# Performance work log

Hardware: AMD Instinct MI355X
Metric: run time of the kernel (lower is better)

Reference implementation:

```python
import jax, jax.numpy as jnp
import numpy as np

DIM = 512
HEADS = 8
HEAD_DIM = DIM // HEADS
MLP_HIDDEN = int(DIM * 4.0)
B, N = 4, 2048
LS_INIT = 1e-5
EPS = 1e-5


def _layernorm(x, w, b):
    mu = jnp.mean(x, axis=-1, keepdims=True)
    var = jnp.mean(jnp.square(x - mu), axis=-1, keepdims=True)
    return (x - mu) * jax.lax.rsqrt(var + EPS) * w + b


def setup_inputs() -> dict:
    key = jax.random.key(0)
    ks = jax.random.split(key, 12)
    s = 0.02
    return {
        "x": jax.random.normal(ks[0], (B, N, DIM), jnp.float32),
        "rel_pos_bias": jax.random.normal(ks[1], (HEADS, N, N), jnp.float32),
        "qkv_w": jax.random.normal(ks[2], (DIM, 3 * DIM), jnp.float32) * s,
        "qkv_b": jnp.zeros((3 * DIM,), jnp.float32),
        "out_w": jax.random.normal(ks[3], (DIM, DIM), jnp.float32) * s,
        "out_b": jnp.zeros((DIM,), jnp.float32),
        "ln1_w": jnp.ones((DIM,), jnp.float32),
        "ln1_b": jnp.zeros((DIM,), jnp.float32),
        "ln2_w": jnp.ones((DIM,), jnp.float32),
        "ln2_b": jnp.zeros((DIM,), jnp.float32),
        "ffn_w1": jax.random.normal(ks[4], (DIM, MLP_HIDDEN), jnp.float32) * s,
        "ffn_b1": jnp.zeros((MLP_HIDDEN,), jnp.float32),
        "ffn_w2": jax.random.normal(ks[5], (MLP_HIDDEN, DIM), jnp.float32) * s,
        "ffn_b2": jnp.zeros((DIM,), jnp.float32),
        "gamma1": jnp.full((DIM,), LS_INIT, jnp.float32),
        "gamma2": jnp.full((DIM,), LS_INIT, jnp.float32),
    }


def reference(x, rel_pos_bias, qkv_w, qkv_b, out_w, out_b, ln1_w, ln1_b,
              ln2_w, ln2_b, ffn_w1, ffn_b1, ffn_w2, ffn_b2, gamma1, gamma2):
    # Pre-norm MHA with relative-position bias
    y = _layernorm(x, ln1_w, ln1_b)                       # [B,N,C]
    qkv = y @ qkv_w + qkv_b                               # [B,N,3C]
    qkv = qkv.reshape(B, N, 3, HEADS, HEAD_DIM)
    q = jnp.transpose(qkv[:, :, 0], (0, 2, 1, 3))         # [B,H,N,D]
    k = jnp.transpose(qkv[:, :, 1], (0, 2, 1, 3))
    v = jnp.transpose(qkv[:, :, 2], (0, 2, 1, 3))
    scale = 1.0 / np.sqrt(HEAD_DIM).astype(np.float32)
    attn = jnp.einsum("bhid,bhjd->bhij", q, k) * scale    # [B,H,N,N]
    attn = attn + rel_pos_bias[None]
    attn = jax.nn.softmax(attn, axis=-1)
    out = jnp.einsum("bhij,bhjd->bhid", attn, v)          # [B,H,N,D]
    out = jnp.transpose(out, (0, 2, 1, 3)).reshape(B, N, DIM)
    out = out @ out_w + out_b
    x = x + out * gamma1                                  # layer scale, no drop-path (eval)
    # FFN with exact GELU
    y2 = _layernorm(x, ln2_w, ln2_b)
    h = jax.nn.gelu(y2 @ ffn_w1 + ffn_b1, approximate=False)
    ffn_out = h @ ffn_w2 + ffn_b2
    x = x + ffn_out * gamma2
    return x
```

## Files before the change

kernel.cpp:

```cpp
#include <hip/hip_runtime.h>
#include <hip/hip_bf16.h>
#include <math.h>

#define SEQ 2048
#define BATCH 4
#define DM 512
#define NH 8
#define HD 64
#define HID 2048
#define ROWS (BATCH * SEQ)

typedef __attribute__((ext_vector_type(8))) short short8;
typedef __attribute__((ext_vector_type(4))) float f32x4;

__device__ __forceinline__ short f2bf(float f) {
    unsigned u = __float_as_uint(f);
    u += 0x7fff + ((u >> 16) & 1);
    return (short)(u >> 16);
}

__device__ __forceinline__ void gl2lds16(const void* g, void* l) {
    __builtin_amdgcn_global_load_lds(
        (const __attribute__((address_space(1))) void*)g,
        (__attribute__((address_space(3))) void*)l, 16, 0, 0);
}

__global__ __launch_bounds__(256) void tcast_all(
    const float* __restrict__ qkv_w, const float* __restrict__ out_w,
    const float* __restrict__ w1, const float* __restrict__ w2,
    short* __restrict__ o_qkv, short* __restrict__ o_out,
    short* __restrict__ o_w1, short* __restrict__ o_w2) {
    __shared__ float tile[32][33];
    int id = blockIdx.x;
    const float* W; short* O; int K, N;
    if (id < 768)       { W = qkv_w; O = o_qkv; K = 512;  N = 1536; }
    else if (id < 1024) { W = out_w; O = o_out; K = 512;  N = 512;  id -= 768; }
    else if (id < 2048) { W = w1;    O = o_w1;  K = 512;  N = 2048; id -= 1024; }
    else                { W = w2;    O = o_w2;  K = 2048; N = 512;  id -= 2048; }
    int tn = N / 32;
    int n0 = (id % tn) * 32, k0 = (id / tn) * 32;
    int tx = threadIdx.x, ty = threadIdx.y;
#pragma unroll
    for (int i = 0; i < 4; ++i)
        tile[ty + i * 8][tx] = W[(size_t)(k0 + ty + i * 8) * N + n0 + tx];
    __syncthreads();
#pragma unroll
    for (int i = 0; i < 4; ++i)
        O[(size_t)(n0 + ty + i * 8) * K + k0 + tx] = f2bf(tile[tx][ty + i * 8]);
}

__global__ __launch_bounds__(256) void bias_prep(const float* __restrict__ bias,
                                                 short* __restrict__ biasP) {
    __shared__ short tl[16][1032];
    int t = threadIdx.x;
    int w = t >> 6, ln = t & 63, quad = ln >> 4, l15 = ln & 15;
    int id = blockIdx.x;
    int half = id & 1;
    int g = (id >> 1) & 127;
    int h = id >> 8;
    const float* src = bias + (size_t)h * SEQ * SEQ + (size_t)g * 16 * SEQ + half * 1024;
#pragma unroll
    for (int i = 0; i < 16; ++i) {
        float4 v = *(const float4*)(src + (size_t)i * SEQ + t * 4);
        float2 lo, hi;
        lo.x = v.x * 1.44269504f; lo.y = v.y * 1.44269504f;
        hi.x = v.z * 1.44269504f; hi.y = v.w * 1.44269504f;
        __hip_bfloat162 l2 = __float22bfloat162_rn(lo);
        __hip_bfloat162 h2 = __float22bfloat162_rn(hi);
        uint2 pp;
        pp.x = *(unsigned*)&l2;
        pp.y = *(unsigned*)&h2;
        *(uint2*)&tl[i][t * 4] = pp;
    }
    __syncthreads();
    int jtbase = half * 16;
#pragma unroll
    for (int u = 0; u < 4; ++u) {
        int jl = w * 4 + u;
        int tau = (h * 128 + g) * 32 + jtbase + jl;
#pragma unroll
        for (int n2 = 0; n2 < 2; ++n2) {
            uint2 a = *(const uint2*)&tl[l15][jl * 64 + n2 * 32 + quad * 4];
            uint2 b = *(const uint2*)&tl[l15][jl * 64 + n2 * 32 + 16 + quad * 4];
            uint4 pp;
            pp.x = a.x; pp.y = a.y; pp.z = b.x; pp.w = b.y;
            *(uint4*)(biasP + (size_t)tau * 1024 + n2 * 512 + ln * 8) = pp;
        }
    }
}

__global__ __launch_bounds__(256) void ln_k(const float* __restrict__ X,
                                            const float* __restrict__ g,
                                            const float* __restrict__ bta,
                                            short* __restrict__ Y) {
    int t = threadIdx.x;
    int wv = t >> 6, ln = t & 63;
    size_t row = (size_t)blockIdx.x * 4 + wv;
    const float* xr = X + row * DM;
    float4 v0 = *(const float4*)(xr + ln * 4);
    float4 v1 = *(const float4*)(xr + 256 + ln * 4);
    float s = v0.x + v0.y + v0.z + v0.w + v1.x + v1.y + v1.z + v1.w;
    float q = v0.x * v0.x + v0.y * v0.y + v0.z * v0.z + v0.w * v0.w +
              v1.x * v1.x + v1.y * v1.y + v1.z * v1.z + v1.w * v1.w;
#pragma unroll
    for (int off = 1; off < 64; off <<= 1) {
        s += __shfl_xor(s, off);
        q += __shfl_xor(q, off);
    }
    float mean = s * (1.0f / 512.0f);
    float var = q * (1.0f / 512.0f) - mean * mean;
    float rstd = rsqrtf(var + 1e-5f);
    int c0 = ln * 4, c1 = 256 + ln * 4;
    ushort4 o0, o1;
    o0.x = (unsigned short)f2bf((v0.x - mean) * rstd * g[c0 + 0] + bta[c0 + 0]);
    o0.y = (unsigned short)f2bf((v0.y - mean) * rstd * g[c0 + 1] + bta[c0 + 1]);
    o0.z = (unsigned short)f2bf((v0.z - mean) * rstd * g[c0 + 2] + bta[c0 + 2]);
    o0.w = (unsigned short)f2bf((v0.w - mean) * rstd * g[c0 + 3] + bta[c0 + 3]);
    o1.x = (unsigned short)f2bf((v1.x - mean) * rstd * g[c1 + 0] + bta[c1 + 0]);
    o1.y = (unsigned short)f2bf((v1.y - mean) * rstd * g[c1 + 1] + bta[c1 + 1]);
    o1.z = (unsigned short)f2bf((v1.z - mean) * rstd * g[c1 + 2] + bta[c1 + 2]);
    o1.w = (unsigned short)f2bf((v1.w - mean) * rstd * g[c1 + 3] + bta[c1 + 3]);
    *(ushort4*)((unsigned short*)Y + row * DM + c0) = o0;
    *(ushort4*)((unsigned short*)Y + row * DM + c1) = o1;
}

template <int EPI, int TN>
__global__ __launch_bounds__(256) void gemm_bt(const short* __restrict__ A,
                                               const short* __restrict__ Bt,
                                               const float* __restrict__ bias,
                                               const float* __restrict__ gamma,
                                               const float* __restrict__ res,
                                               void* __restrict__ Cout,
                                               short* __restrict__ Cout2,
                                               int M, int N, int K) {
    constexpr int NI = TN / 32;
    __shared__ __attribute__((aligned(16))) short As0[128][32];
    __shared__ __attribute__((aligned(16))) short As1[128][32];
    __shared__ __attribute__((aligned(16))) short Bs0[TN][32];
    __shared__ __attribute__((aligned(16))) short Bs1[TN][32];
    int t = threadIdx.x;
    int w = t >> 6, ln = t & 63;
    int quad = ln >> 4, l15 = ln & 15;
    int n0 = blockIdx.x * TN, m0 = blockIdx.y * 128;
    int wm = (w & 1) * 64, wn = (w >> 1) * (TN / 2);

    int srow0 = w * 32 + (ln >> 2);
    int srow1 = srow0 + 16;
    int srowB = w * 16 + (ln >> 2);
    int schunk = (ln & 3) * 8;
    const short* Ag0 = A + (size_t)(m0 + srow0) * K + schunk;
    const short* Ag1 = A + (size_t)(m0 + srow1) * K + schunk;
    const short* Bg0 = Bt + (size_t)(n0 + srow0) * K + schunk;
    const short* Bg1 = Bt + (size_t)(n0 + srow1) * K + schunk;
    const short* BgB = Bt + (size_t)(n0 + srowB) * K + schunk;

    f32x4 acc[4][NI];
#pragma unroll
    for (int i = 0; i < 4; ++i)
#pragma unroll
        for (int j = 0; j < NI; ++j) acc[i][j] = (f32x4){0.f, 0.f, 0.f, 0.f};

    for (int k0 = 0; k0 < K; k0 += 64) {
        __syncthreads();
        gl2lds16(Ag0 + k0, &As0[srow0][schunk]);
        gl2lds16(Ag1 + k0, &As0[srow1][schunk]);
        gl2lds16(Ag0 + k0 + 32, &As1[srow0][schunk]);
        gl2lds16(Ag1 + k0 + 32, &As1[srow1][schunk]);
        if (TN == 128) {
            gl2lds16(Bg0 + k0, &Bs0[srow0 & (TN - 1)][schunk]);
            gl2lds16(Bg1 + k0, &Bs0[srow1 & (TN - 1)][schunk]);
            gl2lds16(Bg0 + k0 + 32, &Bs1[srow0 & (TN - 1)][schunk]);
            gl2lds16(Bg1 + k0 + 32, &Bs1[srow1 & (TN - 1)][schunk]);
        } else {
            gl2lds16(BgB + k0, &Bs0[srowB & (TN - 1)][schunk]);
            gl2lds16(BgB + k0 + 32, &Bs1[srowB & (TN - 1)][schunk]);
        }
        __syncthreads();
        {
            short8 af[4], bf[NI];
#pragma unroll
            for (int mi = 0; mi < 4; ++mi)
                af[mi] = *(const short8*)&As0[wm + mi * 16 + l15][quad * 8];
#pragma unroll
            for (int ni = 0; ni < NI; ++ni)
                bf[ni] = *(const short8*)&Bs0[wn + ni * 16 + l15][quad * 8];
#pragma unroll
            for (int mi = 0; mi < 4; ++mi)
#pragma unroll
                for (int ni = 0; ni < NI; ++ni)
                    acc[mi][ni] = __builtin_amdgcn_mfma_f32_16x16x32_bf16(
                        af[mi], bf[ni], acc[mi][ni], 0, 0, 0);
        }
        {
            short8 af[4], bf[NI];
#pragma unroll
            for (int mi = 0; mi < 4; ++mi)
                af[mi] = *(const short8*)&As1[wm + mi * 16 + l15][quad * 8];
#pragma unroll
            for (int ni = 0; ni < NI; ++ni)
                bf[ni] = *(const short8*)&Bs1[wn + ni * 16 + l15][quad * 8];
#pragma unroll
            for (int mi = 0; mi < 4; ++mi)
#pragma unroll
                for (int ni = 0; ni < NI; ++ni)
                    acc[mi][ni] = __builtin_amdgcn_mfma_f32_16x16x32_bf16(
                        af[mi], bf[ni], acc[mi][ni], 0, 0, 0);
        }
    }

    if (EPI == 3 && n0 >= 1024) {
#pragma unroll
        for (int mi = 0; mi < 4; ++mi) {
#pragma unroll
            for (int ni = 0; ni < NI; ++ni) {
                int col = n0 + wn + ni * 16 + l15;
                int d = col - 1024, hh = d >> 6, dd = d & 63;
                int row0 = m0 + wm + mi * 16 + quad * 4;
                int bb = row0 >> 11, key = row0 & 2047;
                float bs = bias[col];
                ushort4 pk;
                pk.x = (unsigned short)f2bf(acc[mi][ni][0] + bs);
                pk.y = (unsigned short)f2bf(acc[mi][ni][1] + bs);
                pk.z = (unsigned short)f2bf(acc[mi][ni][2] + bs);
                pk.w = (unsigned short)f2bf(acc[mi][ni][3] + bs);
                *(ushort4*)&Cout2[((size_t)(bb * 8 + hh) * 64 + dd) * 2048 + key] = pk;
            }
        }
    } else {
#pragma unroll
        for (int mi = 0; mi < 4; ++mi) {
#pragma unroll
            for (int ni = 0; ni < NI; ++ni) {
#pragma unroll
                for (int r = 0; r < 4; ++r) {
                    int row = m0 + wm + mi * 16 + quad * 4 + r;
                    int col = n0 + wn + ni * 16 + l15;
                    float v = acc[mi][ni][r] + bias[col];
                    if (EPI == 0) {
                        ((short*)Cout)[(size_t)row * N + col] = f2bf(v);
                    } else if (EPI == 1) {
                        float u = v * fmaf(v * v, 0.0713548162f, 1.59576912f);
                        float gg = v / (1.0f + __expf(-u));
                        ((short*)Cout)[(size_t)row * N + col] = f2bf(gg);
                    } else if (EPI == 2) {
                        ((float*)Cout)[(size_t)row * N + col] =
                            fmaf(v, gamma[col], res[(size_t)row * N + col]);
                    } else {
                        float sc = (n0 < 512) ? 0.18033688f : 1.0f;
                        ((short*)Cout)[(size_t)row * 1024 + col] = f2bf(v * sc);
                    }
                }
            }
        }
    }
}

__global__ __launch_bounds__(256, 3) void attn_k(const short* __restrict__ qkv,
                                                 const short* __restrict__ vT,
                                                 const short* __restrict__ biasP,
                                                 short* __restrict__ Aout) {
    __shared__ __attribute__((aligned(16))) short Ks[2][64 * 64];
    __shared__ __attribute__((aligned(16))) short Vs[2][64 * 64];
    __shared__ __attribute__((aligned(16))) short Ps[4][2][16 * 64];
    int t = threadIdx.x;
    int w = t >> 6, ln = t & 63, quad = ln >> 4, l15 = ln & 15;
    int idx = blockIdx.x;
    int h = idx & 7, b = (idx >> 3) & 3, qt = idx >> 5;
    int qb = qt * 128 + w * 16;
    const size_t cbase = (size_t)b * SEQ * 1024;

    const short* qrow0 = qkv + cbase + (size_t)(qb + l15) * 1024 + h * 64;
    const short* qrow1 = qrow0 + (size_t)64 * 1024;
    short8 qf[2][2];
    qf[0][0] = *(const short8*)(qrow0 + quad * 8);
    qf[0][1] = *(const short8*)(qrow0 + 32 + quad * 8);
    qf[1][0] = *(const short8*)(qrow1 + quad * 8);
    qf[1][1] = *(const short8*)(qrow1 + 32 + quad * 8);

    int kr = t >> 3, kc = t & 7;
    int sc = (kc ^ (kr & 7)) * 8;
    const short* kgS = qkv + cbase + 512 + h * 64 + sc;
    const short* vgS = vT + (size_t)(b * 8 + h) * 64 * 2048 + sc;

    int g0 = qt * 8 + w;
    const short* bp0 = biasP + ((size_t)(h * 128 + g0) * 32) * 1024 + ln * 8;
    const short* bp1 = biasP + ((size_t)(h * 128 + g0 + 4) * 32) * 1024 + ln * 8;

    short8 ones;
#pragma unroll
    for (int i = 0; i < 8; ++i) ones[i] = (short)0x3F80;

    f32x4 o[2][4], ol[2];
#pragma unroll
    for (int qg = 0; qg < 2; ++qg) {
#pragma unroll
        for (int db = 0; db < 4; ++db) o[qg][db] = (f32x4){0.f, 0.f, 0.f, 0.f};
        ol[qg] = (f32x4){0.f, 0.f, 0.f, 0.f};
    }

    int sw7 = l15 & 7;

    gl2lds16(kgS,                              &Ks[0][t * 8]);
    gl2lds16(kgS + (size_t)32 * 1024,          &Ks[0][2048 + t * 8]);
    gl2lds16(vgS,                              &Vs[0][t * 8]);
    gl2lds16(vgS + (size_t)32 * 2048,          &Vs[0][2048 + t * 8]);
    uint4 bbc[2][2];
#pragma unroll
    for (int n2 = 0; n2 < 2; ++n2) {
        bbc[0][n2] = *(const uint4*)(bp0 + n2 * 512);
        bbc[1][n2] = *(const uint4*)(bp1 + n2 * 512);
    }

    int cur = 0;
    for (int jt = 0; jt < 32; ++jt) {
        __syncthreads();
        int jn = (jt < 31) ? (jt + 1) : jt;
        int j1 = jn * 64;
        int nxt = cur ^ 1;
        gl2lds16(kgS + (size_t)(j1 + kr) * 1024,      &Ks[nxt][t * 8]);
        gl2lds16(kgS + (size_t)(j1 + 32 + kr) * 1024, &Ks[nxt][2048 + t * 8]);
        gl2lds16(vgS + (size_t)kr * 2048 + j1,        &Vs[nxt][t * 8]);
        gl2lds16(vgS + (size_t)(32 + kr) * 2048 + j1, &Vs[nxt][2048 + t * 8]);

        f32x4 s4[2][4];
#pragma unroll
        for (int ni = 0; ni < 4; ++ni) {
            short8 k0 = *(const short8*)&Ks[cur][(ni * 16 + l15) * 64 + ((quad ^ sw7) * 8)];
            short8 k1 = *(const short8*)&Ks[cur][(ni * 16 + l15) * 64 + (((4 + quad) ^ sw7) * 8)];
#pragma unroll
            for (int qg = 0; qg < 2; ++qg) {
                uint4 bb = bbc[qg][ni >> 1];
                unsigned lo = (ni & 1) ? bb.z : bb.x;
                unsigned hi = (ni & 1) ? bb.w : bb.y;
                f32x4 z;
                z[0] = __uint_as_float(lo << 16);
                z[1] = __uint_as_float(lo & 0xffff0000u);
                z[2] = __uint_as_float(hi << 16);
                z[3] = __uint_as_float(hi & 0xffff0000u);
                z = __builtin_amdgcn_mfma_f32_16x16x32_bf16(k0, qf[qg][0], z, 0, 0, 0);
                s4[qg][ni] = __builtin_amdgcn_mfma_f32_16x16x32_bf16(k1, qf[qg][1], z, 0, 0, 0);
            }
        }
#pragma unroll
        for (int n2 = 0; n2 < 2; ++n2) {
            bbc[0][n2] = *(const uint4*)(bp0 + (size_t)jn * 1024 + n2 * 512);
            bbc[1][n2] = *(const uint4*)(bp1 + (size_t)jn * 1024 + n2 * 512);
        }
#pragma unroll
        for (int qg = 0; qg < 2; ++qg) {
#pragma unroll
            for (int ni = 0; ni < 4; ++ni) {
                float2 plo, phi;
                plo.x = exp2f(s4[qg][ni][0]);
                plo.y = exp2f(s4[qg][ni][1]);
                phi.x = exp2f(s4[qg][ni][2]);
                phi.y = exp2f(s4[qg][ni][3]);
                __hip_bfloat162 l2 = __float22bfloat162_rn(plo);
                __hip_bfloat162 h2 = __float22bfloat162_rn(phi);
                union { uint2 u; } pp;
                pp.u.x = *(unsigned*)&l2;
                pp.u.y = *(unsigned*)&h2;
                int c = ni * 2 + (quad >> 1);
                *(uint2*)&Ps[w][qg][l15 * 64 + ((c ^ sw7) * 8) + (quad & 1) * 4] = pp.u;
            }
        }
#pragma unroll
        for (int kk = 0; kk < 2; ++kk) {
            short8 ap0 = *(const short8*)&Ps[w][0][l15 * 64 + (((kk * 4 + quad) ^ sw7) * 8)];
            short8 ap1 = *(const short8*)&Ps[w][1][l15 * 64 + (((kk * 4 + quad) ^ sw7) * 8)];
#pragma unroll
            for (int db = 0; db < 4; ++db) {
                short8 vv = *(const short8*)&Vs[cur][(db * 16 + l15) * 64 + (((kk * 4 + quad) ^ sw7) * 8)];
                o[0][db] = __builtin_amdgcn_mfma_f32_16x16x32_bf16(ap0, vv, o[0][db], 0, 0, 0);
                o[1][db] = __builtin_amdgcn_mfma_f32_16x16x32_bf16(ap1, vv, o[1][db], 0, 0, 0);
            }
            ol[0] = __builtin_amdgcn_mfma_f32_16x16x32_bf16(ap0, ones, ol[0], 0, 0, 0);
            ol[1] = __builtin_amdgcn_mfma_f32_16x16x32_bf16(ap1, ones, ol[1], 0, 0, 0);
        }
        cur = nxt;
    }
#pragma unroll
    for (int qg = 0; qg < 2; ++qg) {
#pragma unroll
        for (int r = 0; r < 4; ++r) {
            float inv = 1.0f / ol[qg][r];
            int qrow_g = b * SEQ + qb + qg * 64 + quad * 4 + r;
#pragma unroll
            for (int db = 0; db < 4; ++db) {
                Aout[(size_t)qrow_g * DM + h * 64 + db * 16 + l15] =
                    f2bf(o[qg][db][r] * inv);
            }
        }
    }
}

extern "C" void kernel_launch(void* const* d_in, const int* in_sizes, int n_in,
                              void* d_out, int out_size, void* d_ws, size_t ws_size,
                              hipStream_t stream) {
    const float* x      = (const float*)d_in[0];
    const float* bias   = (const float*)d_in[1];
    const float* qkv_w  = (const float*)d_in[2];
    const float* qkv_b  = (const float*)d_in[3];
    const float* out_w  = (const float*)d_in[4];
    const float* out_b  = (const float*)d_in[5];
    const float* ln1_w  = (const float*)d_in[6];
    const float* ln1_b  = (const float*)d_in[7];
    const float* ln2_w  = (const float*)d_in[8];
    const float* ln2_b  = (const float*)d_in[9];
    const float* ffn_w1 = (const float*)d_in[10];
    const float* ffn_b1 = (const float*)d_in[11];
    const float* ffn_w2 = (const float*)d_in[12];
    const float* ffn_b2 = (const float*)d_in[13];
    const float* gamma1 = (const float*)d_in[14];
    const float* gamma2 = (const float*)d_in[15];
    float* out = (float*)d_out;

    short* wqkvT = (short*)d_ws;
    short* woutT = wqkvT + (size_t)1536 * 512;
    short* w1T   = woutT + (size_t)512 * 512;
    short* w2T   = w1T + (size_t)2048 * 512;
    short* y1    = w2T + (size_t)512 * 2048;
    short* qkvB  = y1 + (size_t)ROWS * DM;
    short* vTb   = qkvB + (size_t)ROWS * 1024;
    short* aoutB = vTb + (size_t)32 * 64 * 2048;
    float* x1    = (float*)(aoutB + (size_t)ROWS * DM);
    short* biasPw = (short*)(x1 + (size_t)ROWS * DM);
    short* hB    = qkvB;

    tcast_all<<<3072, dim3(32, 8), 0, stream>>>(qkv_w, out_w, ffn_w1, ffn_w2,
                                                wqkvT, woutT, w1T, w2T);
    bias_prep<<<2048, 256, 0, stream>>>(bias, biasPw);
    ln_k<<<ROWS / 4, 256, 0, stream>>>(x, ln1_w, ln1_b, y1);
    gemm_bt<3, 128><<<dim3(1536 / 128, ROWS / 128), 256, 0, stream>>>(
        y1, wqkvT, qkv_b, nullptr, nullptr, qkvB, vTb, ROWS, 1536, 512);
    attn_k<<<512, 256, 0, stream>>>(qkvB, vTb, biasPw, aoutB);
    gemm_bt<2, 64><<<dim3(512 / 64, ROWS / 128), 256, 0, stream>>>(
        aoutB, woutT, out_b, gamma1, x, x1, nullptr, ROWS, 512, 512);
    ln_k<<<ROWS / 4, 256, 0, stream>>>(x1, ln2_w, ln2_b, y1);
    gemm_bt<1, 128><<<dim3(2048 / 128, ROWS / 128), 256, 0, stream>>>(
        y1, w1T, ffn_b1, nullptr, nullptr, hB, nullptr, ROWS, 2048, 512);
    gemm_bt<2, 64><<<dim3(512 / 64, ROWS / 128), 256, 0, stream>>>(
        hB, w2T, ffn_b2, gamma2, x1, out, nullptr, ROWS, 512, 2048);
}
```

Baseline: 455.7 us.

## Merge bias preprocessing into QKV GEMM kernel via interleaved block roles

```diff
diff --git a/kernel.cpp b/kernel.cpp
--- a/kernel.cpp
+++ b/kernel.cpp
@@ -47,46 +47,6 @@
 #pragma unroll
     for (int i = 0; i < 4; ++i)
         O[(size_t)(n0 + ty + i * 8) * K + k0 + tx] = f2bf(tile[tx][ty + i * 8]);
-}
-
-__global__ __launch_bounds__(256) void bias_prep(const float* __restrict__ bias,
-                                                 short* __restrict__ biasP) {
-    __shared__ short tl[16][1032];
-    int t = threadIdx.x;
-    int w = t >> 6, ln = t & 63, quad = ln >> 4, l15 = ln & 15;
-    int id = blockIdx.x;
-    int half = id & 1;
-    int g = (id >> 1) & 127;
-    int h = id >> 8;
-    const float* src = bias + (size_t)h * SEQ * SEQ + (size_t)g * 16 * SEQ + half * 1024;
-#pragma unroll
-    for (int i = 0; i < 16; ++i) {
-        float4 v = *(const float4*)(src + (size_t)i * SEQ + t * 4);
-        float2 lo, hi;
-        lo.x = v.x * 1.44269504f; lo.y = v.y * 1.44269504f;
-        hi.x = v.z * 1.44269504f; hi.y = v.w * 1.44269504f;
-        __hip_bfloat162 l2 = __float22bfloat162_rn(lo);
-        __hip_bfloat162 h2 = __float22bfloat162_rn(hi);
-        uint2 pp;
-        pp.x = *(unsigned*)&l2;
-        pp.y = *(unsigned*)&h2;
-        *(uint2*)&tl[i][t * 4] = pp;
-    }
-    __syncthreads();
-    int jtbase = half * 16;
-#pragma unroll
-    for (int u = 0; u < 4; ++u) {
-        int jl = w * 4 + u;
-        int tau = (h * 128 + g) * 32 + jtbase + jl;
-#pragma unroll
-        for (int n2 = 0; n2 < 2; ++n2) {
-            uint2 a = *(const uint2*)&tl[l15][jl * 64 + n2 * 32 + quad * 4];
-            uint2 b = *(const uint2*)&tl[l15][jl * 64 + n2 * 32 + 16 + quad * 4];
-            uint4 pp;
-            pp.x = a.x; pp.y = a.y; pp.z = b.x; pp.w = b.y;
-            *(uint4*)(biasP + (size_t)tau * 1024 + n2 * 512 + ln * 8) = pp;
-        }
-    }
 }
 
 __global__ __launch_bounds__(256) void ln_k(const float* __restrict__ X,
@@ -208,48 +168,178 @@
         }
     }
 
-    if (EPI == 3 && n0 >= 1024) {
-#pragma unroll
-        for (int mi = 0; mi < 4; ++mi) {
-#pragma unroll
-            for (int ni = 0; ni < NI; ++ni) {
+#pragma unroll
+    for (int mi = 0; mi < 4; ++mi) {
+#pragma unroll
+        for (int ni = 0; ni < NI; ++ni) {
+#pragma unroll
+            for (int r = 0; r < 4; ++r) {
+                int row = m0 + wm + mi * 16 + quad * 4 + r;
                 int col = n0 + wn + ni * 16 + l15;
-                int d = col - 1024, hh = d >> 6, dd = d & 63;
-                int row0 = m0 + wm + mi * 16 + quad * 4;
-                int bb = row0 >> 11, key = row0 & 2047;
-                float bs = bias[col];
-                ushort4 pk;
-                pk.x = (unsigned short)f2bf(acc[mi][ni][0] + bs);
-                pk.y = (unsigned short)f2bf(acc[mi][ni][1] + bs);
-                pk.z = (unsigned short)f2bf(acc[mi][ni][2] + bs);
-                pk.w = (unsigned short)f2bf(acc[mi][ni][3] + bs);
-                *(ushort4*)&Cout2[((size_t)(bb * 8 + hh) * 64 + dd) * 2048 + key] = pk;
-            }
-        }
-    } else {
-#pragma unroll
-        for (int mi = 0; mi < 4; ++mi) {
-#pragma unroll
-            for (int ni = 0; ni < NI; ++ni) {
-#pragma unroll
-                for (int r = 0; r < 4; ++r) {
-                    int row = m0 + wm + mi * 16 + quad * 4 + r;
+                float v = acc[mi][ni][r] + bias[col];
+                if (EPI == 0) {
+                    ((short*)Cout)[(size_t)row * N + col] = f2bf(v);
+                } else if (EPI == 1) {
+                    float u = v * fmaf(v * v, 0.0713548162f, 1.59576912f);
+                    float gg = v / (1.0f + __expf(-u));
+                    ((short*)Cout)[(size_t)row * N + col] = f2bf(gg);
+                } else {
+                    ((float*)Cout)[(size_t)row * N + col] =
+                        fmaf(v, gamma[col], res[(size_t)row * N + col]);
+                }
+            }
+        }
+    }
+}
+
+__global__ __launch_bounds__(256) void qkvbias_k(
+    const short* __restrict__ A, const short* __restrict__ Bt,
+    const float* __restrict__ qkvb, short* __restrict__ Cout,
+    short* __restrict__ Cout2,
+    const float* __restrict__ bias, short* __restrict__ biasP) {
+    __shared__ __attribute__((aligned(16))) char smem[33024];
+    int bid = blockIdx.x;
+    int grp = bid / 11, sub = bid % 11;
+    int t = threadIdx.x;
+    int w = t >> 6, ln = t & 63;
+    int quad = ln >> 4, l15 = ln & 15;
+
+    if (sub < 3) {
+        typedef short (*tile32)[32];
+        tile32 As0 = (tile32)smem;
+        tile32 As1 = (tile32)(smem + 8192);
+        tile32 Bs0 = (tile32)(smem + 16384);
+        tile32 Bs1 = (tile32)(smem + 24576);
+        const int K = 512, N = 1536;
+        int g = grp * 3 + sub;
+        int n0 = (g % 12) * 128, m0 = (g / 12) * 128;
+        int wm = (w & 1) * 64, wn = (w >> 1) * 64;
+
+        int srow0 = w * 32 + (ln >> 2);
+        int srow1 = srow0 + 16;
+        int schunk = (ln & 3) * 8;
+        const short* Ag0 = A + (size_t)(m0 + srow0) * K + schunk;
+        const short* Ag1 = A + (size_t)(m0 + srow1) * K + schunk;
+        const short* Bg0 = Bt + (size_t)(n0 + srow0) * K + schunk;
+        const short* Bg1 = Bt + (size_t)(n0 + srow1) * K + schunk;
+
+        f32x4 acc[4][4];
+#pragma unroll
+        for (int i = 0; i < 4; ++i)
+#pragma unroll
+            for (int j = 0; j < 4; ++j) acc[i][j] = (f32x4){0.f, 0.f, 0.f, 0.f};
+
+        for (int k0 = 0; k0 < K; k0 += 64) {
+            __syncthreads();
+            gl2lds16(Ag0 + k0, &As0[srow0][schunk]);
+            gl2lds16(Ag1 + k0, &As0[srow1][schunk]);
+            gl2lds16(Ag0 + k0 + 32, &As1[srow0][schunk]);
+            gl2lds16(Ag1 + k0 + 32, &As1[srow1][schunk]);
+            gl2lds16(Bg0 + k0, &Bs0[srow0][schunk]);
+            gl2lds16(Bg1 + k0, &Bs0[srow1][schunk]);
+            gl2lds16(Bg0 + k0 + 32, &Bs1[srow0][schunk]);
+            gl2lds16(Bg1 + k0 + 32, &Bs1[srow1][schunk]);
+            __syncthreads();
+            {
+                short8 af[4], bf[4];
+#pragma unroll
+                for (int mi = 0; mi < 4; ++mi)
+                    af[mi] = *(const short8*)&As0[wm + mi * 16 + l15][quad * 8];
+#pragma unroll
+                for (int ni = 0; ni < 4; ++ni)
+                    bf[ni] = *(const short8*)&Bs0[wn + ni * 16 + l15][quad * 8];
+#pragma unroll
+                for (int mi = 0; mi < 4; ++mi)
+#pragma unroll
+                    for (int ni = 0; ni < 4; ++ni)
+                        acc[mi][ni] = __builtin_amdgcn_mfma_f32_16x16x32_bf16(
+                            af[mi], bf[ni], acc[mi][ni], 0, 0, 0);
+            }
+            {
+                short8 af[4], bf[4];
+#pragma unroll
+                for (int mi = 0; mi < 4; ++mi)
+                    af[mi] = *(const short8*)&As1[wm + mi * 16 + l15][quad * 8];
+#pragma unroll
+                for (int ni = 0; ni < 4; ++ni)
+                    bf[ni] = *(const short8*)&Bs1[wn + ni * 16 + l15][quad * 8];
+#pragma unroll
+                for (int mi = 0; mi < 4; ++mi)
+#pragma unroll
+                    for (int ni = 0; ni < 4; ++ni)
+                        acc[mi][ni] = __builtin_amdgcn_mfma_f32_16x16x32_bf16(
+                            af[mi], bf[ni], acc[mi][ni], 0, 0, 0);
+            }
+        }
+
+        if (n0 >= 1024) {
+#pragma unroll
+            for (int mi = 0; mi < 4; ++mi) {
+#pragma unroll
+                for (int ni = 0; ni < 4; ++ni) {
                     int col = n0 + wn + ni * 16 + l15;
-                    float v = acc[mi][ni][r] + bias[col];
-                    if (EPI == 0) {
-                        ((short*)Cout)[(size_t)row * N + col] = f2bf(v);
-                    } else if (EPI == 1) {
-                        float u = v * fmaf(v * v, 0.0713548162f, 1.59576912f);
-                        float gg = v / (1.0f + __expf(-u));
-                        ((short*)Cout)[(size_t)row * N + col] = f2bf(gg);
-                    } else if (EPI == 2) {
-                        ((float*)Cout)[(size_t)row * N + col] =
-                            fmaf(v, gamma[col], res[(size_t)row * N + col]);
-                    } else {
+                    int d = col - 1024, hh = d >> 6, dd = d & 63;
+                    int row0 = m0 + wm + mi * 16 + quad * 4;
+                    int bb = row0 >> 11, key = row0 & 2047;
+                    float bs = qkvb[col];
+                    ushort4 pk;
+                    pk.x = (unsigned short)f2bf(acc[mi][ni][0] + bs);
+                    pk.y = (unsigned short)f2bf(acc[mi][ni][1] + bs);
+                    pk.z = (unsigned short)f2bf(acc[mi][ni][2] + bs);
+                    pk.w = (unsigned short)f2bf(acc[mi][ni][3] + bs);
+                    *(ushort4*)&Cout2[((size_t)(bb * 8 + hh) * 64 + dd) * 2048 + key] = pk;
+                }
+            }
+        } else {
+#pragma unroll
+            for (int mi = 0; mi < 4; ++mi) {
+#pragma unroll
+                for (int ni = 0; ni < 4; ++ni) {
+#pragma unroll
+                    for (int r = 0; r < 4; ++r) {
+                        int row = m0 + wm + mi * 16 + quad * 4 + r;
+                        int col = n0 + wn + ni * 16 + l15;
+                        float v = acc[mi][ni][r] + qkvb[col];
                         float sc = (n0 < 512) ? 0.18033688f : 1.0f;
-                        ((short*)Cout)[(size_t)row * 1024 + col] = f2bf(v * sc);
+                        Cout[(size_t)row * 1024 + col] = f2bf(v * sc);
                     }
                 }
+            }
+        }
+    } else {
+        typedef short (*tile1032)[1032];
+        tile1032 tl = (tile1032)smem;
+        int id = grp * 8 + (sub - 3);
+        int half = id & 1;
+        int g = (id >> 1) & 127;
+        int h = id >> 8;
+        const float* src = bias + (size_t)h * SEQ * SEQ + (size_t)g * 16 * SEQ + half * 1024;
+#pragma unroll
+        for (int i = 0; i < 16; ++i) {
+            float4 v = *(const float4*)(src + (size_t)i * SEQ + t * 4);
+            float2 lo, hi;
+            lo.x = v.x * 1.44269504f; lo.y = v.y * 1.44269504f;
+            hi.x = v.z * 1.44269504f; hi.y = v.w * 1.44269504f;
+            __hip_bfloat162 l2 = __float22bfloat162_rn(lo);
+            __hip_bfloat162 h2 = __float22bfloat162_rn(hi);
+            uint2 pp;
+            pp.x = *(unsigned*)&l2;
+            pp.y = *(unsigned*)&h2;
+            *(uint2*)&tl[i][t * 4] = pp;
+        }
+        __syncthreads();
+        int jtbase = half * 16;
+#pragma unroll
+        for (int u = 0; u < 4; ++u) {
+            int jl = w * 4 + u;
+            int tau = (h * 128 + g) * 32 + jtbase + jl;
+#pragma unroll
+            for (int n2 = 0; n2 < 2; ++n2) {
+                uint2 a = *(const uint2*)&tl[l15][jl * 64 + n2 * 32 + quad * 4];
+                uint2 b = *(const uint2*)&tl[l15][jl * 64 + n2 * 32 + 16 + quad * 4];
+                uint4 pp;
+                pp.x = a.x; pp.y = a.y; pp.z = b.x; pp.w = b.y;
+                *(uint4*)(biasP + (size_t)tau * 1024 + n2 * 512 + ln * 8) = pp;
             }
         }
     }
@@ -429,10 +519,9 @@
 
     tcast_all<<<3072, dim3(32, 8), 0, stream>>>(qkv_w, out_w, ffn_w1, ffn_w2,
                                                 wqkvT, woutT, w1T, w2T);
-    bias_prep<<<2048, 256, 0, stream>>>(bias, biasPw);
     ln_k<<<ROWS / 4, 256, 0, stream>>>(x, ln1_w, ln1_b, y1);
-    gemm_bt<3, 128><<<dim3(1536 / 128, ROWS / 128), 256, 0, stream>>>(
-        y1, wqkvT, qkv_b, nullptr, nullptr, qkvB, vTb, ROWS, 1536, 512);
+    qkvbias_k<<<2816, 256, 0, stream>>>(y1, wqkvT, qkv_b, qkvB, vTb,
+                                        bias, biasPw);
     attn_k<<<512, 256, 0, stream>>>(qkvB, vTb, biasPw, aoutB);
     gemm_bt<2, 64><<<dim3(512 / 64, ROWS / 128), 256, 0, stream>>>(
         aoutB, woutT, out_b, gamma1, x, x1, nullptr, ROWS, 512, 512);
```

Measured after the change: 435.0 us. -4.5%, faster.
